# Performance work log

Measured on AMD Instinct MI355X. Metric: run time of the kernel, lower is better.

## Reference

```python
import jax, jax.numpy as jnp
import numpy as np

N_NODES = 100000
N_EDGES = 1600000
IN_CH, HID_CH, OUT_CH = 128, 64, 40


def setup_inputs() -> dict:
    key = jax.random.key(0)
    k_x, k_e, k_w1, k_w2 = jax.random.split(key, 4)
    x = jax.random.normal(k_x, (N_NODES, IN_CH), dtype=jnp.float32)
    edge_index = jax.random.randint(k_e, (2, N_EDGES), 0, N_NODES, dtype=jnp.int64)
    # Glorot-ish scaled weights, zero bias (matches GCNConv init convention)
    W1 = jax.random.normal(k_w1, (IN_CH, HID_CH), dtype=jnp.float32) / np.sqrt(IN_CH)
    b1 = jnp.zeros((HID_CH,), dtype=jnp.float32)
    W2 = jax.random.normal(k_w2, (HID_CH, OUT_CH), dtype=jnp.float32) / np.sqrt(HID_CH)
    b2 = jnp.zeros((OUT_CH,), dtype=jnp.float32)
    return {"x": x, "edge_index": edge_index, "W1": W1, "b1": b1, "W2": W2, "b2": b2}


def _gcn_conv(x, edge_index, W, b, n):
    """GCNConv with normalize=True: linear transform, add self-loops,
    symmetric D^-1/2 A D^-1/2 aggregation (source_to_target flow), bias."""
    h = x @ W  # [n, out]
    loops = jnp.arange(n, dtype=edge_index.dtype)
    row = jnp.concatenate([edge_index[0], loops])  # sources
    col = jnp.concatenate([edge_index[1], loops])  # targets
    deg = jax.ops.segment_sum(jnp.ones_like(col, dtype=h.dtype), col, num_segments=n)
    dinv = jnp.where(deg > 0, jax.lax.rsqrt(deg), jnp.zeros_like(deg))
    w = dinv[row] * dinv[col]  # [E+n] per-edge norm
    out = jax.ops.segment_sum(h[row] * w[:, None], col, num_segments=n)  # scatter-add to targets
    return out + b


def reference(x, edge_index, W1, b1, W2, b2):
    # eval mode: F.dropout(p=0.8, training=False) is identity
    n = x.shape[0]
    h = jax.nn.relu(_gcn_conv(x, edge_index, W1, b1, n))
    return _gcn_conv(h, edge_index, W2, b2, n)  # [N, OUT_CH] logits
```

## Files before the change

kernel.cpp:

```cpp
#include <hip/hip_runtime.h>

#define N_NODES 100000
#define N_EDGES 1600000
#define IN_CH   128
#define HID_CH  64
#define OUT_CH  40
#define NBKT    391
#define EPB     4096
#define CAP     6144

using bf16x8 = __attribute__((ext_vector_type(8))) short;
using f32x4  = __attribute__((ext_vector_type(4))) float;

__device__ __forceinline__ float bf2f(unsigned short u) {
    union { unsigned int i; float f; } c; c.i = ((unsigned int)u) << 16; return c.f;
}
__device__ __forceinline__ unsigned short f2bf(float f) {
    union { float f; unsigned int i; } c; c.f = f;
    unsigned int r = c.i + 0x7FFFu + ((c.i >> 16) & 1u);
    return (unsigned short)(r >> 16);
}
__device__ __forceinline__ float4 bf2f4(ushort4 u) {
    return make_float4(bf2f(u.x), bf2f(u.y), bf2f(u.z), bf2f(u.w));
}

__global__ void k_init(int* __restrict__ gcur) {
    int i = blockIdx.x * blockDim.x + threadIdx.x;
    if (i < NBKT) gcur[i] = i * CAP;
}

__global__ void k_prep(const float* __restrict__ W1, const float* __restrict__ W2,
                       unsigned short* __restrict__ W1t, unsigned short* __restrict__ W2t) {
    int stride = gridDim.x * blockDim.x;
    int t0 = blockIdx.x * blockDim.x + threadIdx.x;
    for (int i = t0; i < 64 * 128; i += stride) {
        int n = i >> 7, k = i & 127;
        W1t[i] = f2bf(W1[k * 64 + n]);
    }
    for (int i = t0; i < 48 * 64; i += stride) {
        int n = i >> 6, k = i & 63;
        W2t[i] = f2bf(n < 40 ? W2[k * 40 + n] : 0.0f);
    }
}

__global__ void k_bin(const int* __restrict__ ei, int* __restrict__ gcur,
                      int* __restrict__ ebuf) {
    __shared__ int hist[NBKT];
    __shared__ int lcur[NBKT];
    int tid = threadIdx.x;
    int base = blockIdx.x * EPB;
    int nloc = N_EDGES - base;
    if (nloc > EPB) nloc = EPB;

    for (int i = tid; i < NBKT; i += 256) hist[i] = 0;
    __syncthreads();
    for (int i = tid; i < nloc; i += 256)
        atomicAdd(&hist[ei[N_EDGES + base + i] >> 8], 1);
    __syncthreads();
    for (int i = tid; i < NBKT; i += 256) {
        int h = hist[i];
        lcur[i] = h ? atomicAdd(&gcur[i], h) : 0;
    }
    __syncthreads();
    for (int i = tid; i < nloc; i += 256) {
        int s = ei[base + i];
        int d = ei[N_EDGES + base + i];
        int pos = atomicAdd(&lcur[d >> 8], 1);
        ebuf[pos] = s | ((d & 255) << 20);
    }
}

__global__ void k_node(const int* __restrict__ gcur, const int* __restrict__ ebuf,
                       int* __restrict__ row_start, int* __restrict__ row_end,
                       int* __restrict__ csr_src, float* __restrict__ dinv) {
    __shared__ int cnt[256];
    __shared__ int s[256];
    int tid = threadIdx.x;
    int b = blockIdx.x;
    int node0 = b << 8;
    int lo = b * CAP, hi = gcur[b];

    cnt[tid] = 0;
    __syncthreads();
    for (int e = lo + tid; e < hi; e += 256)
        atomicAdd(&cnt[(unsigned)ebuf[e] >> 20], 1);
    __syncthreads();
    int c = cnt[tid];
    s[tid] = c;
    __syncthreads();
#pragma unroll
    for (int off = 1; off < 256; off <<= 1) {
        int tv = (tid >= off) ? s[tid - off] : 0;
        __syncthreads();
        s[tid] += tv;
        __syncthreads();
    }
    int node = node0 + tid;
    if (node < N_NODES) {
        row_start[node] = lo + s[tid] - c;
        row_end[node]   = lo + s[tid];
        dinv[node] = rsqrtf(1.0f + (float)c);
    }
    __syncthreads();
    cnt[tid] = lo + s[tid] - c;
    __syncthreads();
    for (int e = lo + tid; e < hi; e += 256) {
        int w = ebuf[e];
        int pos = atomicAdd(&cnt[(unsigned)w >> 20], 1);
        csr_src[pos] = w & 0xFFFFF;
    }
}

__global__ __launch_bounds__(256, 4)
void k_gemm1(const float* __restrict__ x, const unsigned short* __restrict__ W1t,
             const float* __restrict__ dinv, unsigned short* __restrict__ h1s) {
    __shared__ unsigned short Al[64 * 136];
    __shared__ unsigned short Bl[64 * 136];
    __shared__ float dl[64];
    int tid = threadIdx.x;
    long long node0 = (long long)blockIdx.x * 64;

    const float4* X = (const float4*)x;
    for (int i = tid; i < 64 * 32; i += 256) {
        int r = i >> 5, c4 = i & 31;
        long long gr = node0 + r;
        if (gr >= N_NODES) gr = N_NODES - 1;
        float4 v = X[gr * 32 + c4];
        *(ushort4*)&Al[r * 136 + c4 * 4] =
            make_ushort4(f2bf(v.x), f2bf(v.y), f2bf(v.z), f2bf(v.w));
    }
    for (int i = tid; i < 64 * 16; i += 256) {
        int n = i >> 4, c8 = i & 15;
        *(ulonglong2*)&Bl[n * 136 + c8 * 8] = *(const ulonglong2*)&W1t[n * 128 + c8 * 8];
    }
    if (tid < 64) {
        long long gr = node0 + tid;
        dl[tid] = dinv[gr < N_NODES ? gr : N_NODES - 1];
    }
    __syncthreads();

    int lane = tid & 63, wave = tid >> 6;
    int quad = lane >> 4, l16 = lane & 15;
    int arow = wave * 16 + l16;
    f32x4 ac0 = {0,0,0,0}, ac1 = {0,0,0,0}, ac2 = {0,0,0,0}, ac3 = {0,0,0,0};

#pragma unroll
    for (int ks = 0; ks < 4; ++ks) {
        int ko = ks * 32 + quad * 8;
        bf16x8 a  = *(const bf16x8*)&Al[arow * 136 + ko];
        bf16x8 b0 = *(const bf16x8*)&Bl[( 0 + l16) * 136 + ko];
        bf16x8 b1 = *(const bf16x8*)&Bl[(16 + l16) * 136 + ko];
        bf16x8 b2 = *(const bf16x8*)&Bl[(32 + l16) * 136 + ko];
        bf16x8 b3 = *(const bf16x8*)&Bl[(48 + l16) * 136 + ko];
        ac0 = __builtin_amdgcn_mfma_f32_16x16x32_bf16(a, b0, ac0, 0, 0, 0);
        ac1 = __builtin_amdgcn_mfma_f32_16x16x32_bf16(a, b1, ac1, 0, 0, 0);
        ac2 = __builtin_amdgcn_mfma_f32_16x16x32_bf16(a, b2, ac2, 0, 0, 0);
        ac3 = __builtin_amdgcn_mfma_f32_16x16x32_bf16(a, b3, ac3, 0, 0, 0);
    }

#pragma unroll
    for (int r = 0; r < 4; ++r) {
        int rl = wave * 16 + quad * 4 + r;
        long long grow = node0 + rl;
        if (grow < N_NODES) {
            float dd = dl[rl];
            h1s[grow * 64 +  0 + l16] = f2bf(ac0[r] * dd);
            h1s[grow * 64 + 16 + l16] = f2bf(ac1[r] * dd);
            h1s[grow * 64 + 32 + l16] = f2bf(ac2[r] * dd);
            h1s[grow * 64 + 48 + l16] = f2bf(ac3[r] * dd);
        }
    }
}

__global__ void k_agg1(const int* __restrict__ row_start, const int* __restrict__ row_end,
                       const int* __restrict__ csr_src,
                       const unsigned short* __restrict__ h1s, const float* __restrict__ dinv,
                       float* __restrict__ a1) {
    int idx = blockIdx.x * blockDim.x + threadIdx.x;
    int node = idx >> 4;
    int cg = idx & 15;
    if (node >= N_NODES) return;
    int beg = row_start[node];
    int end = row_end[node];
    const ushort4* H = (const ushort4*)h1s;
    float4 acc = bf2f4(H[(long long)node * 16 + cg]);
    int e = beg;
    for (; e + 3 < end; e += 4) {
        int s0 = csr_src[e];
        int s1 = csr_src[e + 1];
        int s2 = csr_src[e + 2];
        int s3 = csr_src[e + 3];
        float4 v0 = bf2f4(H[(long long)s0 * 16 + cg]);
        float4 v1 = bf2f4(H[(long long)s1 * 16 + cg]);
        float4 v2 = bf2f4(H[(long long)s2 * 16 + cg]);
        float4 v3 = bf2f4(H[(long long)s3 * 16 + cg]);
        acc.x += (v0.x + v1.x) + (v2.x + v3.x);
        acc.y += (v0.y + v1.y) + (v2.y + v3.y);
        acc.z += (v0.z + v1.z) + (v2.z + v3.z);
        acc.w += (v0.w + v1.w) + (v2.w + v3.w);
    }
    for (; e < end; ++e) {
        float4 v = bf2f4(H[(long long)csr_src[e] * 16 + cg]);
        acc.x += v.x; acc.y += v.y; acc.z += v.z; acc.w += v.w;
    }
    float dd = dinv[node];
    acc.x *= dd; acc.y *= dd; acc.z *= dd; acc.w *= dd;
    ((float4*)a1)[(long long)node * 16 + cg] = acc;
}

__global__ __launch_bounds__(256, 4)
void k_gemm2(const float* __restrict__ a1, const unsigned short* __restrict__ W2t,
             const float* __restrict__ b1, const float* __restrict__ dinv,
             unsigned short* __restrict__ h2s) {
    __shared__ unsigned short Al[64 * 72];
    __shared__ unsigned short Bl[48 * 72];
    __shared__ float dl[64];
    int tid = threadIdx.x;
    long long node0 = (long long)blockIdx.x * 64;

    const float4* A = (const float4*)a1;
    int c4 = tid & 15;
    float4 bb = ((const float4*)b1)[c4];
    for (int i = tid; i < 64 * 16; i += 256) {
        int r = i >> 4;
        long long gr = node0 + r;
        if (gr >= N_NODES) gr = N_NODES - 1;
        float4 v = A[gr * 16 + c4];
        v.x = fmaxf(v.x + bb.x, 0.f); v.y = fmaxf(v.y + bb.y, 0.f);
        v.z = fmaxf(v.z + bb.z, 0.f); v.w = fmaxf(v.w + bb.w, 0.f);
        *(ushort4*)&Al[r * 72 + c4 * 4] =
            make_ushort4(f2bf(v.x), f2bf(v.y), f2bf(v.z), f2bf(v.w));
    }
    for (int i = tid; i < 48 * 8; i += 256) {
        int n = i >> 3, c8 = i & 7;
        *(ulonglong2*)&Bl[n * 72 + c8 * 8] = *(const ulonglong2*)&W2t[n * 64 + c8 * 8];
    }
    if (tid < 64) {
        long long gr = node0 + tid;
        dl[tid] = dinv[gr < N_NODES ? gr : N_NODES - 1];
    }
    __syncthreads();

    int lane = tid & 63, wave = tid >> 6;
    int quad = lane >> 4, l16 = lane & 15;
    int arow = wave * 16 + l16;
    f32x4 ac0 = {0,0,0,0}, ac1 = {0,0,0,0}, ac2 = {0,0,0,0};

#pragma unroll
    for (int ks = 0; ks < 2; ++ks) {
        int ko = ks * 32 + quad * 8;
        bf16x8 a  = *(const bf16x8*)&Al[arow * 72 + ko];
        bf16x8 b0 = *(const bf16x8*)&Bl[( 0 + l16) * 72 + ko];
        bf16x8 b1v = *(const bf16x8*)&Bl[(16 + l16) * 72 + ko];
        bf16x8 b2 = *(const bf16x8*)&Bl[(32 + l16) * 72 + ko];
        ac0 = __builtin_amdgcn_mfma_f32_16x16x32_bf16(a, b0, ac0, 0, 0, 0);
        ac1 = __builtin_amdgcn_mfma_f32_16x16x32_bf16(a, b1v, ac1, 0, 0, 0);
        ac2 = __builtin_amdgcn_mfma_f32_16x16x32_bf16(a, b2, ac2, 0, 0, 0);
    }

#pragma unroll
    for (int r = 0; r < 4; ++r) {
        int rl = wave * 16 + quad * 4 + r;
        long long grow = node0 + rl;
        if (grow < N_NODES) {
            float dd = dl[rl];
            h2s[grow * 40 +  0 + l16] = f2bf(ac0[r] * dd);
            h2s[grow * 40 + 16 + l16] = f2bf(ac1[r] * dd);
            if (l16 < 8) h2s[grow * 40 + 32 + l16] = f2bf(ac2[r] * dd);
        }
    }
}

__global__ void k_agg2(const int* __restrict__ row_start, const int* __restrict__ row_end,
                       const int* __restrict__ csr_src,
                       const unsigned short* __restrict__ h2s, const float* __restrict__ dinv,
                       const float* __restrict__ b2, float* __restrict__ out) {
    int idx = blockIdx.x * blockDim.x + threadIdx.x;
    int node = idx >> 4;
    int cg = idx & 15;
    if (node >= N_NODES || cg >= 10) return;
    int beg = row_start[node];
    int end = row_end[node];
    const ushort4* H = (const ushort4*)h2s;
    float4 acc = bf2f4(H[(long long)node * 10 + cg]);
    int e = beg;
    for (; e + 3 < end; e += 4) {
        int s0 = csr_src[e];
        int s1 = csr_src[e + 1];
        int s2 = csr_src[e + 2];
        int s3 = csr_src[e + 3];
        float4 v0 = bf2f4(H[(long long)s0 * 10 + cg]);
        float4 v1 = bf2f4(H[(long long)s1 * 10 + cg]);
        float4 v2 = bf2f4(H[(long long)s2 * 10 + cg]);
        float4 v3 = bf2f4(H[(long long)s3 * 10 + cg]);
        acc.x += (v0.x + v1.x) + (v2.x + v3.x);
        acc.y += (v0.y + v1.y) + (v2.y + v3.y);
        acc.z += (v0.z + v1.z) + (v2.z + v3.z);
        acc.w += (v0.w + v1.w) + (v2.w + v3.w);
    }
    for (; e < end; ++e) {
        float4 v = bf2f4(H[(long long)csr_src[e] * 10 + cg]);
        acc.x += v.x; acc.y += v.y; acc.z += v.z; acc.w += v.w;
    }
    float dd = dinv[node];
    float4 b = ((const float4*)b2)[cg];
    acc.x = acc.x * dd + b.x;
    acc.y = acc.y * dd + b.y;
    acc.z = acc.z * dd + b.z;
    acc.w = acc.w * dd + b.w;
    ((float4*)out)[(long long)node * 10 + cg] = acc;
}

extern "C" void kernel_launch(void* const* d_in, const int* in_sizes, int n_in,
                              void* d_out, int out_size, void* d_ws, size_t ws_size,
                              hipStream_t stream) {
    const float* x  = (const float*)d_in[0];
    const int*   ei = (const int*)d_in[1];
    const float* W1 = (const float*)d_in[2];
    const float* b1 = (const float*)d_in[3];
    const float* W2 = (const float*)d_in[4];
    const float* b2 = (const float*)d_in[5];
    float* out = (float*)d_out;

    float* a1 = (float*)d_ws;
    unsigned short* hbuf = (unsigned short*)(a1 + 64LL * N_NODES);
    int* ebuf      = (int*)(hbuf + 64LL * N_NODES);
    int* csr_src   = ebuf + NBKT * CAP;
    int* row_start = csr_src + NBKT * CAP;
    int* row_end   = row_start + N_NODES;
    int* gcur      = row_end + N_NODES;
    float* dinv    = (float*)(gcur + 400);
    unsigned short* W1t = (unsigned short*)(dinv + N_NODES);
    unsigned short* W2t = W1t + 64 * 128;

    const int B = 256;
    const int g16 = (N_NODES * 16 + B - 1) / B;
    const int gRows = (N_NODES + 63) / 64;

    k_init<<<2, B, 0, stream>>>(gcur);
    k_prep<<<8, B, 0, stream>>>(W1, W2, W1t, W2t);
    k_bin<<<(N_EDGES + EPB - 1) / EPB, B, 0, stream>>>(ei, gcur, ebuf);
    k_node<<<NBKT, B, 0, stream>>>(gcur, ebuf, row_start, row_end, csr_src, dinv);

    k_gemm1<<<gRows, B, 0, stream>>>(x, W1t, dinv, hbuf);
    k_agg1<<<g16, B, 0, stream>>>(row_start, row_end, csr_src, hbuf, dinv, a1);

    k_gemm2<<<gRows, B, 0, stream>>>(a1, W2t, b1, dinv, hbuf);
    k_agg2<<<g16, B, 0, stream>>>(row_start, row_end, csr_src, hbuf, dinv, b2, out);
}
```

Before: 234.8 us.

## Merge setup kernels, vectorize binning, fuse bias/ReLU into agg1 with bf16 output

```diff
diff --git a/kernel.cpp b/kernel.cpp
--- a/kernel.cpp
+++ b/kernel.cpp
@@ -24,15 +24,12 @@
     return make_float4(bf2f(u.x), bf2f(u.y), bf2f(u.z), bf2f(u.w));
 }
 
-__global__ void k_init(int* __restrict__ gcur) {
-    int i = blockIdx.x * blockDim.x + threadIdx.x;
-    if (i < NBKT) gcur[i] = i * CAP;
-}
-
-__global__ void k_prep(const float* __restrict__ W1, const float* __restrict__ W2,
-                       unsigned short* __restrict__ W1t, unsigned short* __restrict__ W2t) {
+__global__ void k_setup(const float* __restrict__ W1, const float* __restrict__ W2,
+                        unsigned short* __restrict__ W1t, unsigned short* __restrict__ W2t,
+                        int* __restrict__ gcur) {
     int stride = gridDim.x * blockDim.x;
     int t0 = blockIdx.x * blockDim.x + threadIdx.x;
+    if (t0 < NBKT) gcur[t0] = t0 * CAP;
     for (int i = t0; i < 64 * 128; i += stride) {
         int n = i >> 7, k = i & 127;
         W1t[i] = f2bf(W1[k * 64 + n]);
@@ -51,22 +48,33 @@
     int base = blockIdx.x * EPB;
     int nloc = N_EDGES - base;
     if (nloc > EPB) nloc = EPB;
+    int n4 = nloc >> 2;
+    const int4* S4 = (const int4*)(ei + base);
+    const int4* D4 = (const int4*)(ei + N_EDGES + base);
 
     for (int i = tid; i < NBKT; i += 256) hist[i] = 0;
     __syncthreads();
-    for (int i = tid; i < nloc; i += 256)
-        atomicAdd(&hist[ei[N_EDGES + base + i] >> 8], 1);
+    for (int i = tid; i < n4; i += 256) {
+        int4 d = D4[i];
+        atomicAdd(&hist[d.x >> 8], 1);
+        atomicAdd(&hist[d.y >> 8], 1);
+        atomicAdd(&hist[d.z >> 8], 1);
+        atomicAdd(&hist[d.w >> 8], 1);
+    }
     __syncthreads();
     for (int i = tid; i < NBKT; i += 256) {
         int h = hist[i];
         lcur[i] = h ? atomicAdd(&gcur[i], h) : 0;
     }
     __syncthreads();
-    for (int i = tid; i < nloc; i += 256) {
-        int s = ei[base + i];
-        int d = ei[N_EDGES + base + i];
-        int pos = atomicAdd(&lcur[d >> 8], 1);
-        ebuf[pos] = s | ((d & 255) << 20);
+    for (int i = tid; i < n4; i += 256) {
+        int4 s = S4[i];
+        int4 d = D4[i];
+        int p;
+        p = atomicAdd(&lcur[d.x >> 8], 1); ebuf[p] = s.x | ((d.x & 255) << 20);
+        p = atomicAdd(&lcur[d.y >> 8], 1); ebuf[p] = s.y | ((d.y & 255) << 20);
+        p = atomicAdd(&lcur[d.z >> 8], 1); ebuf[p] = s.z | ((d.z & 255) << 20);
+        p = atomicAdd(&lcur[d.w >> 8], 1); ebuf[p] = s.w | ((d.w & 255) << 20);
     }
 }
 
@@ -79,10 +87,19 @@
     int b = blockIdx.x;
     int node0 = b << 8;
     int lo = b * CAP, hi = gcur[b];
+    int n = hi - lo, n4 = n >> 2;
+    const int4* E4 = (const int4*)(ebuf + lo);
 
     cnt[tid] = 0;
     __syncthreads();
-    for (int e = lo + tid; e < hi; e += 256)
+    for (int i = tid; i < n4; i += 256) {
+        int4 w = E4[i];
+        atomicAdd(&cnt[(unsigned)w.x >> 20], 1);
+        atomicAdd(&cnt[(unsigned)w.y >> 20], 1);
+        atomicAdd(&cnt[(unsigned)w.z >> 20], 1);
+        atomicAdd(&cnt[(unsigned)w.w >> 20], 1);
+    }
+    for (int e = lo + (n4 << 2) + tid; e < hi; e += 256)
         atomicAdd(&cnt[(unsigned)ebuf[e] >> 20], 1);
     __syncthreads();
     int c = cnt[tid];
@@ -104,10 +121,18 @@
     __syncthreads();
     cnt[tid] = lo + s[tid] - c;
     __syncthreads();
-    for (int e = lo + tid; e < hi; e += 256) {
+    for (int i = tid; i < n4; i += 256) {
+        int4 w = E4[i];
+        int p;
+        p = atomicAdd(&cnt[(unsigned)w.x >> 20], 1); csr_src[p] = w.x & 0xFFFFF;
+        p = atomicAdd(&cnt[(unsigned)w.y >> 20], 1); csr_src[p] = w.y & 0xFFFFF;
+        p = atomicAdd(&cnt[(unsigned)w.z >> 20], 1); csr_src[p] = w.z & 0xFFFFF;
+        p = atomicAdd(&cnt[(unsigned)w.w >> 20], 1); csr_src[p] = w.w & 0xFFFFF;
+    }
+    for (int e = lo + (n4 << 2) + tid; e < hi; e += 256) {
         int w = ebuf[e];
-        int pos = atomicAdd(&cnt[(unsigned)w >> 20], 1);
-        csr_src[pos] = w & 0xFFFFF;
+        int p = atomicAdd(&cnt[(unsigned)w >> 20], 1);
+        csr_src[p] = w & 0xFFFFF;
     }
 }
 
@@ -130,8 +155,8 @@
             make_ushort4(f2bf(v.x), f2bf(v.y), f2bf(v.z), f2bf(v.w));
     }
     for (int i = tid; i < 64 * 16; i += 256) {
-        int n = i >> 4, c8 = i & 15;
-        *(ulonglong2*)&Bl[n * 136 + c8 * 8] = *(const ulonglong2*)&W1t[n * 128 + c8 * 8];
+        int nn = i >> 4, c8 = i & 15;
+        *(ulonglong2*)&Bl[nn * 136 + c8 * 8] = *(const ulonglong2*)&W1t[nn * 128 + c8 * 8];
     }
     if (tid < 64) {
         long long gr = node0 + tid;
@@ -175,65 +200,76 @@
 __global__ void k_agg1(const int* __restrict__ row_start, const int* __restrict__ row_end,
                        const int* __restrict__ csr_src,
                        const unsigned short* __restrict__ h1s, const float* __restrict__ dinv,
-                       float* __restrict__ a1) {
+                       const float* __restrict__ b1, unsigned short* __restrict__ a1b) {
     int idx = blockIdx.x * blockDim.x + threadIdx.x;
     int node = idx >> 4;
     int cg = idx & 15;
     if (node >= N_NODES) return;
-    int beg = row_start[node];
-    int end = row_end[node];
+    int e = row_start[node];
+    int f = row_end[node];
     const ushort4* H = (const ushort4*)h1s;
     float4 acc = bf2f4(H[(long long)node * 16 + cg]);
-    int e = beg;
-    for (; e + 3 < end; e += 4) {
+    float4 acc2 = {0.f, 0.f, 0.f, 0.f};
+    while (f - e >= 8) {
         int s0 = csr_src[e];
         int s1 = csr_src[e + 1];
         int s2 = csr_src[e + 2];
         int s3 = csr_src[e + 3];
+        int t0 = csr_src[f - 4];
+        int t1 = csr_src[f - 3];
+        int t2 = csr_src[f - 2];
+        int t3 = csr_src[f - 1];
         float4 v0 = bf2f4(H[(long long)s0 * 16 + cg]);
         float4 v1 = bf2f4(H[(long long)s1 * 16 + cg]);
         float4 v2 = bf2f4(H[(long long)s2 * 16 + cg]);
         float4 v3 = bf2f4(H[(long long)s3 * 16 + cg]);
-        acc.x += (v0.x + v1.x) + (v2.x + v3.x);
-        acc.y += (v0.y + v1.y) + (v2.y + v3.y);
-        acc.z += (v0.z + v1.z) + (v2.z + v3.z);
-        acc.w += (v0.w + v1.w) + (v2.w + v3.w);
-    }
-    for (; e < end; ++e) {
+        float4 u0 = bf2f4(H[(long long)t0 * 16 + cg]);
+        float4 u1 = bf2f4(H[(long long)t1 * 16 + cg]);
+        float4 u2 = bf2f4(H[(long long)t2 * 16 + cg]);
+        float4 u3 = bf2f4(H[(long long)t3 * 16 + cg]);
+        acc.x  += (v0.x + v1.x) + (v2.x + v3.x);
+        acc.y  += (v0.y + v1.y) + (v2.y + v3.y);
+        acc.z  += (v0.z + v1.z) + (v2.z + v3.z);
+        acc.w  += (v0.w + v1.w) + (v2.w + v3.w);
+        acc2.x += (u0.x + u1.x) + (u2.x + u3.x);
+        acc2.y += (u0.y + u1.y) + (u2.y + u3.y);
+        acc2.z += (u0.z + u1.z) + (u2.z + u3.z);
+        acc2.w += (u0.w + u1.w) + (u2.w + u3.w);
+        e += 4; f -= 4;
+    }
+    for (; e < f; ++e) {
         float4 v = bf2f4(H[(long long)csr_src[e] * 16 + cg]);
         acc.x += v.x; acc.y += v.y; acc.z += v.z; acc.w += v.w;
     }
+    acc.x += acc2.x; acc.y += acc2.y; acc.z += acc2.z; acc.w += acc2.w;
     float dd = dinv[node];
-    acc.x *= dd; acc.y *= dd; acc.z *= dd; acc.w *= dd;
-    ((float4*)a1)[(long long)node * 16 + cg] = acc;
+    float4 bb = ((const float4*)b1)[cg];
+    float rx = fmaxf(acc.x * dd + bb.x, 0.f);
+    float ry = fmaxf(acc.y * dd + bb.y, 0.f);
+    float rz = fmaxf(acc.z * dd + bb.z, 0.f);
+    float rw = fmaxf(acc.w * dd + bb.w, 0.f);
+    ((ushort4*)a1b)[(long long)node * 16 + cg] =
+        make_ushort4(f2bf(rx), f2bf(ry), f2bf(rz), f2bf(rw));
 }
 
 __global__ __launch_bounds__(256, 4)
-void k_gemm2(const float* __restrict__ a1, const unsigned short* __restrict__ W2t,
-             const float* __restrict__ b1, const float* __restrict__ dinv,
-             unsigned short* __restrict__ h2s) {
+void k_gemm2(const unsigned short* __restrict__ a1b, const unsigned short* __restrict__ W2t,
+             const float* __restrict__ dinv, unsigned short* __restrict__ h2s) {
     __shared__ unsigned short Al[64 * 72];
     __shared__ unsigned short Bl[48 * 72];
     __shared__ float dl[64];
     int tid = threadIdx.x;
     long long node0 = (long long)blockIdx.x * 64;
 
-    const float4* A = (const float4*)a1;
-    int c4 = tid & 15;
-    float4 bb = ((const float4*)b1)[c4];
-    for (int i = tid; i < 64 * 16; i += 256) {
-        int r = i >> 4;
+    for (int i = tid; i < 64 * 8; i += 256) {
+        int r = i >> 3, c8 = i & 7;
         long long gr = node0 + r;
         if (gr >= N_NODES) gr = N_NODES - 1;
-        float4 v = A[gr * 16 + c4];
-        v.x = fmaxf(v.x + bb.x, 0.f); v.y = fmaxf(v.y + bb.y, 0.f);
-        v.z = fmaxf(v.z + bb.z, 0.f); v.w = fmaxf(v.w + bb.w, 0.f);
-        *(ushort4*)&Al[r * 72 + c4 * 4] =
-            make_ushort4(f2bf(v.x), f2bf(v.y), f2bf(v.z), f2bf(v.w));
+        *(ulonglong2*)&Al[r * 72 + c8 * 8] = *(const ulonglong2*)&a1b[gr * 64 + c8 * 8];
     }
     for (int i = tid; i < 48 * 8; i += 256) {
-        int n = i >> 3, c8 = i & 7;
-        *(ulonglong2*)&Bl[n * 72 + c8 * 8] = *(const ulonglong2*)&W2t[n * 64 + c8 * 8];
+        int nn = i >> 3, c8 = i & 7;
+        *(ulonglong2*)&Bl[nn * 72 + c8 * 8] = *(const ulonglong2*)&W2t[nn * 64 + c8 * 8];
     }
     if (tid < 64) {
         long long gr = node0 + tid;
@@ -279,29 +315,43 @@
     int node = idx >> 4;
     int cg = idx & 15;
     if (node >= N_NODES || cg >= 10) return;
-    int beg = row_start[node];
-    int end = row_end[node];
+    int e = row_start[node];
+    int f = row_end[node];
     const ushort4* H = (const ushort4*)h2s;
     float4 acc = bf2f4(H[(long long)node * 10 + cg]);
-    int e = beg;
-    for (; e + 3 < end; e += 4) {
+    float4 acc2 = {0.f, 0.f, 0.f, 0.f};
+    while (f - e >= 8) {
         int s0 = csr_src[e];
         int s1 = csr_src[e + 1];
         int s2 = csr_src[e + 2];
         int s3 = csr_src[e + 3];
+        int t0 = csr_src[f - 4];
+        int t1 = csr_src[f - 3];
+        int t2 = csr_src[f - 2];
+        int t3 = csr_src[f - 1];
         float4 v0 = bf2f4(H[(long long)s0 * 10 + cg]);
         float4 v1 = bf2f4(H[(long long)s1 * 10 + cg]);
         float4 v2 = bf2f4(H[(long long)s2 * 10 + cg]);
         float4 v3 = bf2f4(H[(long long)s3 * 10 + cg]);
-        acc.x += (v0.x + v1.x) + (v2.x + v3.x);
-        acc.y += (v0.y + v1.y) + (v2.y + v3.y);
-        acc.z += (v0.z + v1.z) + (v2.z + v3.z);
-        acc.w += (v0.w + v1.w) + (v2.w + v3.w);
-    }
-    for (; e < end; ++e) {
+        float4 u0 = bf2f4(H[(long long)t0 * 10 + cg]);
+        float4 u1 = bf2f4(H[(long long)t1 * 10 + cg]);
+        float4 u2 = bf2f4(H[(long long)t2 * 10 + cg]);
+        float4 u3 = bf2f4(H[(long long)t3 * 10 + cg]);
+        acc.x  += (v0.x + v1.x) + (v2.x + v3.x);
+        acc.y  += (v0.y + v1.y) + (v2.y + v3.y);
+        acc.z  += (v0.z + v1.z) + (v2.z + v3.z);
+        acc.w  += (v0.w + v1.w) + (v2.w + v3.w);
+        acc2.x += (u0.x + u1.x) + (u2.x + u3.x);
+        acc2.y += (u0.y + u1.y) + (u2.y + u3.y);
+        acc2.z += (u0.z + u1.z) + (u2.z + u3.z);
+        acc2.w += (u0.w + u1.w) + (u2.w + u3.w);
+        e += 4; f -= 4;
+    }
+    for (; e < f; ++e) {
         float4 v = bf2f4(H[(long long)csr_src[e] * 10 + cg]);
         acc.x += v.x; acc.y += v.y; acc.z += v.z; acc.w += v.w;
     }
+    acc.x += acc2.x; acc.y += acc2.y; acc.z += acc2.z; acc.w += acc2.w;
     float dd = dinv[node];
     float4 b = ((const float4*)b2)[cg];
     acc.x = acc.x * dd + b.x;
@@ -322,9 +372,9 @@
     const float* b2 = (const float*)d_in[5];
     float* out = (float*)d_out;
 
-    float* a1 = (float*)d_ws;
-    unsigned short* hbuf = (unsigned short*)(a1 + 64LL * N_NODES);
-    int* ebuf      = (int*)(hbuf + 64LL * N_NODES);
+    unsigned short* hbuf = (unsigned short*)d_ws;
+    unsigned short* a1b  = hbuf + 64LL * N_NODES;
+    int* ebuf      = (int*)(a1b + 64LL * N_NODES);
     int* csr_src   = ebuf + NBKT * CAP;
     int* row_start = csr_src + NBKT * CAP;
     int* row_end   = row_start + N_NODES;
@@ -337,14 +387,13 @@
     const int g16 = (N_NODES * 16 + B - 1) / B;
     const int gRows = (N_NODES + 63) / 64;
 
-    k_init<<<2, B, 0, stream>>>(gcur);
-    k_prep<<<8, B, 0, stream>>>(W1, W2, W1t, W2t);
+    k_setup<<<34, B, 0, stream>>>(W1, W2, W1t, W2t, gcur);
     k_bin<<<(N_EDGES + EPB - 1) / EPB, B, 0, stream>>>(ei, gcur, ebuf);
     k_node<<<NBKT, B, 0, stream>>>(gcur, ebuf, row_start, row_end, csr_src, dinv);
 
     k_gemm1<<<gRows, B, 0, stream>>>(x, W1t, dinv, hbuf);
-    k_agg1<<<g16, B, 0, stream>>>(row_start, row_end, csr_src, hbuf, dinv, a1);
-
-    k_gemm2<<<gRows, B, 0, stream>>>(a1, W2t, b1, dinv, hbuf);
+    k_agg1<<<g16, B, 0, stream>>>(row_start, row_end, csr_src, hbuf, dinv, b1, a1b);
+
+    k_gemm2<<<gRows, B, 0, stream>>>(a1b, W2t, dinv, hbuf);
     k_agg2<<<g16, B, 0, stream>>>(row_start, row_end, csr_src, hbuf, dinv, b2, out);
 }
```

Result: faster. 226.5 us (-3.5%).
